# Optimization experiments

Measured on AMD Instinct MI355X. Metric: run time of the kernel, lower is better.

## Reference

```python
import jax, jax.numpy as jnp
import numpy as np

NUM_NODES = 100000
NUM_EDGES = 50000
NUM_CONN = 800000
IN_DIM = 256
HIDDEN = 128
EDGE_ATTR_DIM = 17
LN_EPS = 1e-5


def setup_inputs() -> dict:
    key = jax.random.key(0)
    k1, k2, k3, kw1, kb1, kg, kbeta, kw2, kb2 = jax.random.split(key, 9)
    node_features = jax.random.normal(k1, (NUM_NODES, IN_DIM), dtype=jnp.float32)
    nodes = jax.random.randint(k2, (NUM_CONN,), 0, NUM_NODES, dtype=jnp.int64)
    edges = jax.random.randint(k3, (NUM_CONN,), 0, NUM_EDGES, dtype=jnp.int64)
    hyperedge_index = jnp.stack([nodes, edges], axis=0)
    # MLP params (Linear(in,hid) -> LayerNorm -> ReLU -> Dropout(eval:identity) -> Linear(hid,out))
    W1 = jax.random.normal(kw1, (IN_DIM, HIDDEN), dtype=jnp.float32) * (1.0 / np.sqrt(IN_DIM))
    b1 = jax.random.normal(kb1, (HIDDEN,), dtype=jnp.float32) * 0.01
    ln_g = jnp.ones((HIDDEN,), dtype=jnp.float32)
    ln_b = jnp.zeros((HIDDEN,), dtype=jnp.float32)
    W2 = jax.random.normal(kw2, (HIDDEN, EDGE_ATTR_DIM), dtype=jnp.float32) * (1.0 / np.sqrt(HIDDEN))
    b2 = jax.random.normal(kb2, (EDGE_ATTR_DIM,), dtype=jnp.float32) * 0.01
    return {"node_features": node_features, "hyperedge_index": hyperedge_index,
            "W1": W1, "b1": b1, "ln_g": ln_g, "ln_b": ln_b, "W2": W2, "b2": b2}


def reference(node_features, hyperedge_index, W1, b1, ln_g, ln_b, W2, b2):
    nodes = hyperedge_index[0]
    edges = hyperedge_index[1]
    # indices are in-range by construction (torch valid_mask is all-True here)
    gathered = node_features[nodes]                         # [num_conn, in_dim]
    summed = jax.ops.segment_sum(gathered, edges, num_segments=NUM_EDGES)
    counts = jax.ops.segment_sum(jnp.ones(edges.shape, node_features.dtype), edges,
                                 num_segments=NUM_EDGES)
    edge_features = summed / jnp.clip(counts, 1.0)[:, None]  # mean aggregation
    # decoder MLP (dropout inactive in eval)
    h = edge_features @ W1 + b1
    mu = jnp.mean(h, axis=-1, keepdims=True)
    var = jnp.mean(jnp.square(h - mu), axis=-1, keepdims=True)
    h = (h - mu) * jax.lax.rsqrt(var + LN_EPS) * ln_g + ln_b
    h = jax.nn.relu(h)
    return h @ W2 + b2                                      # [num_edges, edge_attr_dim]
```

## Files before the change

### kernel.cpp

```cpp
#include <hip/hip_runtime.h>
#include <hip/hip_bf16.h>
#include <stdint.h>

#define NUM_NODES 100000
#define NUM_EDGES 50000
#define NUM_CONN  800000
#define IN_DIM    256
#define HIDDEN    128
#define EDGE_DIM  17
#define PAD       64

typedef __bf16 bf16x8 __attribute__((ext_vector_type(8)));
typedef float  f32x4  __attribute__((ext_vector_type(4)));


__global__ void prep_kernel(const float* __restrict__ W1, const float* __restrict__ W2,
                            __bf16* __restrict__ w1f, __bf16* __restrict__ w2f,
                            int* __restrict__ counts) {
    int i = blockIdx.x * 256 + threadIdx.x;
    if (i < NUM_EDGES) counts[i] = 0;
    if (i < 4096) {
        int lane = i & 63, t = (i >> 6) & 7, kc2 = i >> 9;
        int m = lane & 15, q = lane >> 4;
        int n = t * 16 + m;
        int kbase = kc2 * 32 + q * 8;
        __bf16* dst = w1f + (size_t)i * 8;
        #pragma unroll
        for (int ki = 0; ki < 8; ++ki)
            dst[ki] = (__bf16)W1[(size_t)(kbase + ki) * HIDDEN + n];
    } else if (i < 4608) {
        int f = i - 4096;
        int lane = f & 63, t = (f >> 6) & 1, ks = f >> 7;
        int m = lane & 15, q = lane >> 4;
        int n = t * 16 + m;
        int kbase = ks * 32 + q * 8;
        __bf16* dst = w2f + (size_t)f * 8;
        #pragma unroll
        for (int ki = 0; ki < 8; ++ki)
            dst[ki] = (n < EDGE_DIM) ? (__bf16)W2[(size_t)(kbase + ki) * EDGE_DIM + n]
                                     : (__bf16)0.0f;
    }
}

#define FRONT_BLOCKS 2346
__global__ __launch_bounds__(256) void front_kernel(const int* __restrict__ idx,
        int* __restrict__ counts, int* __restrict__ slots,
        const float* __restrict__ nf, const __bf16* __restrict__ w1f,
        __bf16* __restrict__ pbf) {
    if (blockIdx.x % 3 != 2) {
        int b = blockIdx.x - blockIdx.x / 3;
        int i = b * 256 + threadIdx.x;
        if (i < NUM_CONN / 2) {
            int2 vn = ((const int2*)idx)[i];
            int2 ve = ((const int2*)(idx + NUM_CONN))[i];
            int p0 = atomicAdd(&counts[ve.x], 1);
            if (p0 < PAD) slots[(size_t)ve.x * PAD + p0] = vn.x;
            int p1 = atomicAdd(&counts[ve.y], 1);
            if (p1 < PAD) slots[(size_t)ve.y * PAD + p1] = vn.y;
        }
        return;
    }
    const int p_idx = blockIdx.x / 3;
    const int wave = threadIdx.x >> 6;
    const int lane = threadIdx.x & 63;
    const int m = lane & 15, q = lane >> 4;
    const int rowbase = p_idx * 128 + wave * 32;
    const bf16x8* __restrict__ frag = (const bf16x8*)w1f;

    f32x4 acc[2][8];
    #pragma unroll
    for (int mt = 0; mt < 2; ++mt)
        #pragma unroll
        for (int t = 0; t < 8; ++t) acc[mt][t] = (f32x4){0.f, 0.f, 0.f, 0.f};

    const float* ap[2];
    #pragma unroll
    for (int mt = 0; mt < 2; ++mt) {
        int r = rowbase + mt * 16 + m;
        if (r >= NUM_NODES) r = NUM_NODES - 1;
        ap[mt] = nf + (size_t)r * IN_DIM + q * 8;
    }

    #pragma unroll
    for (int kc2 = 0; kc2 < 8; ++kc2) {
        bf16x8 b[8];
        #pragma unroll
        for (int t = 0; t < 8; ++t) b[t] = frag[(kc2 * 8 + t) * 64 + lane];
        #pragma unroll
        for (int mt = 0; mt < 2; ++mt) {
            float4 f0 = *(const float4*)(ap[mt] + kc2 * 32);
            float4 f1 = *(const float4*)(ap[mt] + kc2 * 32 + 4);
            bf16x8 a;
            a[0] = (__bf16)f0.x; a[1] = (__bf16)f0.y;
            a[2] = (__bf16)f0.z; a[3] = (__bf16)f0.w;
            a[4] = (__bf16)f1.x; a[5] = (__bf16)f1.y;
            a[6] = (__bf16)f1.z; a[7] = (__bf16)f1.w;
            #pragma unroll
            for (int t = 0; t < 8; ++t)
                acc[mt][t] = __builtin_amdgcn_mfma_f32_16x16x32_bf16(a, b[t], acc[mt][t], 0, 0, 0);
        }
    }

    #pragma unroll
    for (int mt = 0; mt < 2; ++mt) {
        int ob = rowbase + mt * 16 + q * 4;
        #pragma unroll
        for (int t = 0; t < 8; ++t)
            #pragma unroll
            for (int r = 0; r < 4; ++r) {
                int orow = ob + r;
                if (orow < NUM_NODES)
                    pbf[(size_t)orow * HIDDEN + t * 16 + m] = (__bf16)acc[mt][t][r];
            }
    }
}

__global__ __launch_bounds__(256) void edge_kernel(const uint4* __restrict__ p4,
        const int* __restrict__ counts, const int* __restrict__ slots,
        const float* __restrict__ b1, const float* __restrict__ ln_g,
        const float* __restrict__ ln_b, const __bf16* __restrict__ w2f,
        const float* __restrict__ b2, float* __restrict__ out) {
    __shared__ __align__(16) uint4 lds_r[256];
    const int wave = threadIdx.x >> 6;
    const int lane = threadIdx.x & 63;
    const int g = lane & 15, ge = lane >> 4;
    const int el = wave * 4 + ge;
    const int e = blockIdx.x * 16 + el;

    const int c = counts[e];
    const int cc = c < PAD ? c : PAD;
    const float inv = 1.0f / (float)(c > 0 ? c : 1);

    float acc[8];
    #pragma unroll
    for (int d = 0; d < 8; ++d) acc[d] = 0.f;

    for (int c0 = 0; c0 < cc; c0 += 16) {
        int slv = slots[(size_t)e * PAD + c0 + g];
        int lim = cc - c0; if (lim > 16) lim = 16;
        if (lim == 16) {
            #pragma unroll
            for (int k0 = 0; k0 < 16; k0 += 4) {
                uint4 u[4];
                #pragma unroll
                for (int k = 0; k < 4; ++k) {
                    int nd = __shfl(slv, ge * 16 + k0 + k, 64);
                    u[k] = p4[(size_t)nd * 16 + g];
                }
                #pragma unroll
                for (int k = 0; k < 4; ++k) {
                    acc[0] += __uint_as_float(u[k].x << 16);
                    acc[1] += __uint_as_float(u[k].x & 0xffff0000u);
                    acc[2] += __uint_as_float(u[k].y << 16);
                    acc[3] += __uint_as_float(u[k].y & 0xffff0000u);
                    acc[4] += __uint_as_float(u[k].z << 16);
                    acc[5] += __uint_as_float(u[k].z & 0xffff0000u);
                    acc[6] += __uint_as_float(u[k].w << 16);
                    acc[7] += __uint_as_float(u[k].w & 0xffff0000u);
                }
            }
        } else {
            for (int k0 = 0; k0 < lim; k0 += 4) {
                uint4 u[4];
                unsigned okm[4];
                #pragma unroll
                for (int k = 0; k < 4; ++k) {
                    int nd = __shfl(slv, ge * 16 + k0 + k, 64);
                    nd = ((unsigned)nd < NUM_NODES) ? nd : 0;
                    u[k] = p4[(size_t)nd * 16 + g];
                    okm[k] = (k0 + k < lim) ? 0xffffffffu : 0u;
                }
                #pragma unroll
                for (int k = 0; k < 4; ++k) {
                    uint4 v = u[k];
                    v.x &= okm[k]; v.y &= okm[k]; v.z &= okm[k]; v.w &= okm[k];
                    acc[0] += __uint_as_float(v.x << 16);
                    acc[1] += __uint_as_float(v.x & 0xffff0000u);
                    acc[2] += __uint_as_float(v.y << 16);
                    acc[3] += __uint_as_float(v.y & 0xffff0000u);
                    acc[4] += __uint_as_float(v.z << 16);
                    acc[5] += __uint_as_float(v.z & 0xffff0000u);
                    acc[6] += __uint_as_float(v.w << 16);
                    acc[7] += __uint_as_float(v.w & 0xffff0000u);
                }
            }
        }
    }

    float4 bA = ((const float4*)b1)[2 * g];
    float4 bB = ((const float4*)b1)[2 * g + 1];
    float h[8];
    h[0] = acc[0] * inv + bA.x; h[1] = acc[1] * inv + bA.y;
    h[2] = acc[2] * inv + bA.z; h[3] = acc[3] * inv + bA.w;
    h[4] = acc[4] * inv + bB.x; h[5] = acc[5] * inv + bB.y;
    h[6] = acc[6] * inv + bB.z; h[7] = acc[7] * inv + bB.w;

    float s = 0.f;
    #pragma unroll
    for (int d = 0; d < 8; ++d) s += h[d];
    #pragma unroll
    for (int off = 8; off > 0; off >>= 1) s += __shfl_xor(s, off, 64);
    float mu = s * (1.0f / 128.0f);

    float dv[8], vv = 0.f;
    #pragma unroll
    for (int d = 0; d < 8; ++d) { dv[d] = h[d] - mu; vv += dv[d] * dv[d]; }
    #pragma unroll
    for (int off = 8; off > 0; off >>= 1) vv += __shfl_xor(vv, off, 64);
    float rs = rsqrtf(vv * (1.0f / 128.0f) + 1e-5f);

    float4 gA = ((const float4*)ln_g)[2 * g];
    float4 gB = ((const float4*)ln_g)[2 * g + 1];
    float4 eA = ((const float4*)ln_b)[2 * g];
    float4 eB = ((const float4*)ln_b)[2 * g + 1];
    float gg[8] = {gA.x, gA.y, gA.z, gA.w, gB.x, gB.y, gB.z, gB.w};
    float ee[8] = {eA.x, eA.y, eA.z, eA.w, eB.x, eB.y, eB.z, eB.w};
    union { __bf16 b[8]; uint4 u; } pk;
    #pragma unroll
    for (int d = 0; d < 8; ++d) {
        float r = dv[d] * rs * gg[d] + ee[d];
        pk.b[d] = (__bf16)(r > 0.f ? r : 0.f);
    }
    lds_r[el * 16 + g] = pk.u;
    __syncthreads();

    if (wave == 0) {
        const int m = lane & 15, q = lane >> 4;
        const __bf16* lr = (const __bf16*)lds_r;
        const bf16x8* fw = (const bf16x8*)w2f;
        f32x4 a0 = (f32x4){0.f, 0.f, 0.f, 0.f};
        f32x4 a1 = (f32x4){0.f, 0.f, 0.f, 0.f};
        #pragma unroll
        for (int ks = 0; ks < 4; ++ks) {
            bf16x8 a = *(const bf16x8*)(lr + m * 128 + ks * 32 + q * 8);
            a0 = __builtin_amdgcn_mfma_f32_16x16x32_bf16(a, fw[(ks * 2 + 0) * 64 + lane], a0, 0, 0, 0);
            a1 = __builtin_amdgcn_mfma_f32_16x16x32_bf16(a, fw[(ks * 2 + 1) * 64 + lane], a1, 0, 0, 0);
        }
        int rowb = blockIdx.x * 16 + q * 4;
        float bm = b2[m];
        float b16 = b2[16];
        #pragma unroll
        for (int r = 0; r < 4; ++r) {
            out[(size_t)(rowb + r) * EDGE_DIM + m] = a0[r] + bm;
            if (m == 0) out[(size_t)(rowb + r) * EDGE_DIM + 16] = a1[r] + b16;
        }
    }
}

extern "C" void kernel_launch(void* const* d_in, const int* in_sizes, int n_in,
                              void* d_out, int out_size, void* d_ws, size_t ws_size,
                              hipStream_t stream) {
    const float* nf  = (const float*)d_in[0];
    const int*   idx = (const int*)d_in[1];
    const float* W1  = (const float*)d_in[2];
    const float* b1  = (const float*)d_in[3];
    const float* g   = (const float*)d_in[4];
    const float* be  = (const float*)d_in[5];
    const float* W2  = (const float*)d_in[6];
    const float* b2  = (const float*)d_in[7];
    float* out = (float*)d_out;

    char* ws = (char*)d_ws;
    __bf16* P      = (__bf16*)ws;
    int*    counts = (int*)(ws + 25600000);
    int*    slots  = (int*)(ws + 25800000);
    __bf16* W1F    = (__bf16*)(ws + 38600000);
    __bf16* W2F    = (__bf16*)(ws + 38665536);

    prep_kernel<<<196, 256, 0, stream>>>(W1, W2, W1F, W2F, counts);
    front_kernel<<<FRONT_BLOCKS, 256, 0, stream>>>(idx, counts, slots, nf, W1F, P);
    edge_kernel<<<NUM_EDGES / 16, 256, 0, stream>>>((const uint4*)P, counts, slots,
                                                    b1, g, be, W2F, b2, out);
}
```

Baseline: 252.7 us.

## Retile node projection GEMM with LDS-staged W1 halves and batched index atomics

The front kernel now splits the node projection into 256-row tiles. Each block computes half of the hidden columns and stages that W1 half in LDS instead of reading fragments from global memory. The bucketing blocks each handle 8 connections per thread and issue their atomics back to back, and a runtime stride check supports both int32 and int64 index layouts. Block interleaving changes to 1 scatter block per 9. Each node row is now read twice, once per column half, in exchange for smaller register tiles and better occupancy.

```diff
diff --git a/kernel.cpp b/kernel.cpp
--- a/kernel.cpp
+++ b/kernel.cpp
@@ -42,40 +42,70 @@
     }
 }
 
-#define FRONT_BLOCKS 2346
-__global__ __launch_bounds__(256) void front_kernel(const int* __restrict__ idx,
-        int* __restrict__ counts, int* __restrict__ slots,
+#define FRONT_BLOCKS 3519
+__global__ __launch_bounds__(256, 4) void front_kernel(const int* __restrict__ idx,
+        int stride, int* __restrict__ counts, int* __restrict__ slots,
         const float* __restrict__ nf, const __bf16* __restrict__ w1f,
         __bf16* __restrict__ pbf) {
-    if (blockIdx.x % 3 != 2) {
-        int b = blockIdx.x - blockIdx.x / 3;
-        int i = b * 256 + threadIdx.x;
-        if (i < NUM_CONN / 2) {
-            int2 vn = ((const int2*)idx)[i];
-            int2 ve = ((const int2*)(idx + NUM_CONN))[i];
-            int p0 = atomicAdd(&counts[ve.x], 1);
-            if (p0 < PAD) slots[(size_t)ve.x * PAD + p0] = vn.x;
-            int p1 = atomicAdd(&counts[ve.y], 1);
-            if (p1 < PAD) slots[(size_t)ve.y * PAD + p1] = vn.y;
+    __shared__ __align__(16) __bf16 lds_w[16384];
+    if (blockIdx.x % 9 == 4) {
+        int b = blockIdx.x / 9;
+        long c0 = ((long)b * 256 + threadIdx.x) * 8;
+        if (c0 < NUM_CONN) {
+            int nd[8], ed[8];
+            if (stride == 2) {
+                #pragma unroll
+                for (int k = 0; k < 4; ++k) {
+                    int4 vn = ((const int4*)idx)[c0 / 2 + k];
+                    int4 ve = ((const int4*)(idx + 2 * NUM_CONN))[c0 / 2 + k];
+                    nd[2 * k] = vn.x; nd[2 * k + 1] = vn.z;
+                    ed[2 * k] = ve.x; ed[2 * k + 1] = ve.z;
+                }
+            } else {
+                #pragma unroll
+                for (int k = 0; k < 8; ++k) {
+                    nd[k] = idx[c0 + k];
+                    ed[k] = idx[NUM_CONN + c0 + k];
+                }
+            }
+            int pos[8];
+            #pragma unroll
+            for (int k = 0; k < 8; ++k) pos[k] = atomicAdd(&counts[ed[k]], 1);
+            #pragma unroll
+            for (int k = 0; k < 8; ++k)
+                if (pos[k] < PAD) slots[(size_t)ed[k] * PAD + pos[k]] = nd[k];
         }
         return;
     }
-    const int p_idx = blockIdx.x / 3;
+    const int p = blockIdx.x - blockIdx.x / 9 - (blockIdx.x % 9 > 4 ? 1 : 0);
+    const int rt = p >> 1;
+    const int ch = p & 1;
+    {
+        const uint4* src = (const uint4*)w1f;
+        uint4* dst = (uint4*)lds_w;
+        #pragma unroll
+        for (int i = threadIdx.x; i < 2048; i += 256) {
+            int kc2 = i >> 8, tt = (i >> 6) & 3, lane = i & 63;
+            dst[i] = src[(kc2 * 8 + ch * 4 + tt) * 64 + lane];
+        }
+    }
+    __syncthreads();
+
     const int wave = threadIdx.x >> 6;
     const int lane = threadIdx.x & 63;
     const int m = lane & 15, q = lane >> 4;
-    const int rowbase = p_idx * 128 + wave * 32;
-    const bf16x8* __restrict__ frag = (const bf16x8*)w1f;
-
-    f32x4 acc[2][8];
-    #pragma unroll
-    for (int mt = 0; mt < 2; ++mt)
-        #pragma unroll
-        for (int t = 0; t < 8; ++t) acc[mt][t] = (f32x4){0.f, 0.f, 0.f, 0.f};
-
-    const float* ap[2];
-    #pragma unroll
-    for (int mt = 0; mt < 2; ++mt) {
+    const int rowbase = rt * 256 + wave * 64;
+    const bf16x8* frag = (const bf16x8*)lds_w;
+
+    f32x4 acc[4][4];
+    #pragma unroll
+    for (int mt = 0; mt < 4; ++mt)
+        #pragma unroll
+        for (int tt = 0; tt < 4; ++tt) acc[mt][tt] = (f32x4){0.f, 0.f, 0.f, 0.f};
+
+    const float* ap[4];
+    #pragma unroll
+    for (int mt = 0; mt < 4; ++mt) {
         int r = rowbase + mt * 16 + m;
         if (r >= NUM_NODES) r = NUM_NODES - 1;
         ap[mt] = nf + (size_t)r * IN_DIM + q * 8;
@@ -83,11 +113,11 @@
 
     #pragma unroll
     for (int kc2 = 0; kc2 < 8; ++kc2) {
-        bf16x8 b[8];
-        #pragma unroll
-        for (int t = 0; t < 8; ++t) b[t] = frag[(kc2 * 8 + t) * 64 + lane];
-        #pragma unroll
-        for (int mt = 0; mt < 2; ++mt) {
+        bf16x8 b[4];
+        #pragma unroll
+        for (int tt = 0; tt < 4; ++tt) b[tt] = frag[(kc2 * 4 + tt) * 64 + lane];
+        #pragma unroll
+        for (int mt = 0; mt < 4; ++mt) {
             float4 f0 = *(const float4*)(ap[mt] + kc2 * 32);
             float4 f1 = *(const float4*)(ap[mt] + kc2 * 32 + 4);
             bf16x8 a;
@@ -96,22 +126,24 @@
             a[4] = (__bf16)f1.x; a[5] = (__bf16)f1.y;
             a[6] = (__bf16)f1.z; a[7] = (__bf16)f1.w;
             #pragma unroll
-            for (int t = 0; t < 8; ++t)
-                acc[mt][t] = __builtin_amdgcn_mfma_f32_16x16x32_bf16(a, b[t], acc[mt][t], 0, 0, 0);
-        }
-    }
-
-    #pragma unroll
-    for (int mt = 0; mt < 2; ++mt) {
+            for (int tt = 0; tt < 4; ++tt)
+                acc[mt][tt] = __builtin_amdgcn_mfma_f32_16x16x32_bf16(a, b[tt], acc[mt][tt], 0, 0, 0);
+        }
+    }
+
+    #pragma unroll
+    for (int mt = 0; mt < 4; ++mt) {
         int ob = rowbase + mt * 16 + q * 4;
         #pragma unroll
-        for (int t = 0; t < 8; ++t)
+        for (int tt = 0; tt < 4; ++tt) {
+            int col = (ch * 4 + tt) * 16 + m;
             #pragma unroll
             for (int r = 0; r < 4; ++r) {
                 int orow = ob + r;
                 if (orow < NUM_NODES)
-                    pbf[(size_t)orow * HIDDEN + t * 16 + m] = (__bf16)acc[mt][t][r];
+                    pbf[(size_t)orow * HIDDEN + col] = (__bf16)acc[mt][tt][r];
             }
+        }
     }
 }
 
@@ -267,8 +299,10 @@
     __bf16* W1F    = (__bf16*)(ws + 38600000);
     __bf16* W2F    = (__bf16*)(ws + 38665536);
 
+    int stride = (in_sizes[1] == 2 * NUM_CONN) ? 1 : 2;
+
     prep_kernel<<<196, 256, 0, stream>>>(W1, W2, W1F, W2F, counts);
-    front_kernel<<<FRONT_BLOCKS, 256, 0, stream>>>(idx, counts, slots, nf, W1F, P);
+    front_kernel<<<FRONT_BLOCKS, 256, 0, stream>>>(idx, stride, counts, slots, nf, W1F, P);
     edge_kernel<<<NUM_EDGES / 16, 256, 0, stream>>>((const uint4*)P, counts, slots,
                                                     b1, g, be, W2F, b2, out);
 }
```

Result: slower. 261.4 us (+3.5%).
